# Kernel tuning notes

Measured on AMD Instinct MI355X. Metric: run time of the kernel, lower is better.

## Reference

```python
import jax, jax.numpy as jnp
import numpy as np

B, T, K, F, H, LH, OUT = 256, 90, 17, 2, 64, 512, 57
N_PER = T * K  # 1530 nodes per graph
IN1 = K * (H + F)  # 1122
CONNS = [[15,13],[13,11],[16,14],[14,12],[11,12],[5,11],[6,12],[5,6],[5,7],[6,8],[7,9],[8,10],[1,2],[0,1],[0,2],[1,3],[2,4],[3,5],[4,6]]

def _build_edge_index():
    temporal = np.array([[i, i + K] for i in range(N_PER - K)], dtype=np.int64).T
    structural = np.array([[a + i * K, b + i * K] for a, b in CONNS for i in range(T)], dtype=np.int64).T
    e = np.concatenate([temporal, structural], axis=1)
    e = np.concatenate([e, e[::-1]], axis=1)  # bidirectional
    e = np.concatenate([e + g * N_PER for g in range(B)], axis=1)  # batch offsets
    return jnp.asarray(e)


def setup_inputs() -> dict:
    key = jax.random.key(0)
    ks = jax.random.split(key, 40)
    def n(i, shape, s=0.05):
        return jax.random.normal(ks[i], shape, dtype=jnp.float32) * s
    inp = {
        'x': jax.random.normal(ks[0], (B * N_PER, F), dtype=jnp.float32),
        'edge_index': _build_edge_index(),
        'gat1_W': n(1, (F, H), 0.3), 'gat1_asrc': n(2, (H,), 0.3), 'gat1_adst': n(3, (H,), 0.3), 'gat1_b': n(4, (H,)),
        'bn1_g': jnp.ones((H,), jnp.float32), 'bn1_b': jnp.zeros((H,), jnp.float32),
        'gat2_W': n(5, (H, H), 0.1), 'gat2_asrc': n(6, (H,), 0.3), 'gat2_adst': n(7, (H,), 0.3), 'gat2_b': n(8, (H,)),
        'bn2_g': jnp.ones((H,), jnp.float32), 'bn2_b': jnp.zeros((H,), jnp.float32),
        'l1f_wih': n(9, (4 * LH, IN1)), 'l1f_whh': n(10, (4 * LH, LH)), 'l1f_bih': n(11, (4 * LH,)), 'l1f_bhh': n(12, (4 * LH,)),
        'l1b_wih': n(13, (4 * LH, IN1)), 'l1b_whh': n(14, (4 * LH, LH)), 'l1b_bih': n(15, (4 * LH,)), 'l1b_bhh': n(16, (4 * LH,)),
        'l2f_wih': n(17, (4 * LH, 2 * LH)), 'l2f_whh': n(18, (4 * LH, LH)), 'l2f_bih': n(19, (4 * LH,)), 'l2f_bhh': n(20, (4 * LH,)),
        'l2b_wih': n(21, (4 * LH, 2 * LH)), 'l2b_whh': n(22, (4 * LH, LH)), 'l2b_bih': n(23, (4 * LH,)), 'l2b_bhh': n(24, (4 * LH,)),
        'h1_w': n(25, (2 * LH, 256)), 'h1_b': n(26, (256,)),
        'h2_w': n(27, (256, OUT)), 'h2_b': n(28, (OUT,)),
    }
    return inp


def _gat(x, src, dst, W, a_src, a_dst, b):
    # PyG GATConv, heads=1, self-loops included in src/dst
    N = x.shape[0]
    xp = x @ W  # [N, H]
    e = jax.nn.leaky_relu((xp @ a_src)[src] + (xp @ a_dst)[dst], 0.2)  # [E]
    m = jax.ops.segment_max(e, dst, num_segments=N)
    w = jnp.exp(e - m[dst])
    den = jax.ops.segment_sum(w, dst, num_segments=N)
    alpha = w / den[dst]
    out = jax.ops.segment_sum(xp[src] * alpha[:, None], dst, num_segments=N)
    return out + b


def _bn(x, g, b):
    mu = x.mean(0)
    var = ((x - mu) ** 2).mean(0)
    return g * (x - mu) * jax.lax.rsqrt(var + 1e-5) + b


def _lstm_dir(x, wih, whh, bih, bhh):
    Bn, Hh = x.shape[0], whh.shape[1]
    def step(carry, xt):
        h, c = carry
        z = xt @ wih.T + h @ whh.T + bih + bhh
        i, f, g, o = jnp.split(z, 4, axis=-1)  # torch gate order
        c = jax.nn.sigmoid(f) * c + jax.nn.sigmoid(i) * jnp.tanh(g)
        h = jax.nn.sigmoid(o) * jnp.tanh(c)
        return (h, c), h
    h0 = jnp.zeros((Bn, Hh), x.dtype)
    _, hs = jax.lax.scan(step, (h0, h0), jnp.swapaxes(x, 0, 1))
    return jnp.swapaxes(hs, 0, 1)


def _bilstm(x, wf_ih, wf_hh, bf_ih, bf_hh, wb_ih, wb_hh, bb_ih, bb_hh):
    fwd = _lstm_dir(x, wf_ih, wf_hh, bf_ih, bf_hh)
    bwd = _lstm_dir(x[:, ::-1], wb_ih, wb_hh, bb_ih, bb_hh)[:, ::-1]
    return jnp.concatenate([fwd, bwd], axis=-1)


def reference(x, edge_index,
              gat1_W, gat1_asrc, gat1_adst, gat1_b, bn1_g, bn1_b,
              gat2_W, gat2_asrc, gat2_adst, gat2_b, bn2_g, bn2_b,
              l1f_wih, l1f_whh, l1f_bih, l1f_bhh, l1b_wih, l1b_whh, l1b_bih, l1b_bhh,
              l2f_wih, l2f_whh, l2f_bih, l2f_bhh, l2b_wih, l2b_whh, l2b_bih, l2b_bhh,
              h1_w, h1_b, h2_w, h2_b):
    N = x.shape[0]
    sl = jnp.arange(N)
    src = jnp.concatenate([edge_index[0], sl])  # add self loops (GATConv default)
    dst = jnp.concatenate([edge_index[1], sl])
    h = jax.nn.relu(_bn(_gat(x, src, dst, gat1_W, gat1_asrc, gat1_adst, gat1_b), bn1_g, bn1_b))
    h = jax.nn.relu(_bn(_gat(h, src, dst, gat2_W, gat2_asrc, gat2_adst, gat2_b), bn2_g, bn2_b))
    feats = jnp.concatenate([h, x], axis=1).reshape(B, T, IN1)  # [B, 90, 1122]
    o = _bilstm(feats, l1f_wih, l1f_whh, l1f_bih, l1f_bhh, l1b_wih, l1b_whh, l1b_bih, l1b_bhh)
    o = _bilstm(o, l2f_wih, l2f_whh, l2f_bih, l2f_bhh, l2b_wih, l2b_whh, l2b_bih, l2b_bhh)
    o = jax.nn.relu(o @ h1_w + h1_b) @ h2_w + h2_b  # [B, 90, 57]
    return o
```

## Files before the change

kernel.cpp:

```cpp
#include <hip/hip_runtime.h>
#include <cstdint>
#include <cstddef>

#define B_    256
#define T_    90
#define K_    17
#define NPER  1530
#define NN    (B_*NPER)
#define H_    64
#define LH    512
#define G4    2048
#define IN1   1122
#define IN1P  1152
#define SEQR  (B_*T_)
#define OUT_  57

typedef unsigned short u16;
typedef __attribute__((ext_vector_type(8))) short short8;
typedef __attribute__((ext_vector_type(4))) float f32x4;

__device__ __forceinline__ float b2f(u16 u){ union{unsigned i; float f;} x; x.i=((unsigned)u)<<16; return x.f; }
__device__ __forceinline__ u16 f2b(float f){ union{float f; unsigned i;} x; x.f=f; unsigned r=x.i+0x7fffu+((x.i>>16)&1u); return (u16)(r>>16); }
__device__ __forceinline__ float sigm(float v){ return 1.f/(1.f+__expf(-v)); }
__device__ __forceinline__ float tanh_(float v){ return 2.f*sigm(2.f*v)-1.f; }

__global__ __launch_bounds__(256)
void stg_sentinel(float* __restrict__ out, int n){
  int i=blockIdx.x*256+threadIdx.x;
  if(i<n) out[i]=123.0f;
}

__global__ __launch_bounds__(256)
void stg_permute_w(const float* __restrict__ src, u16* __restrict__ dst, int Ks, int Kd){
  size_t idx=(size_t)blockIdx.x*256+threadIdx.x;
  int rn=(int)(idx/Kd), kk=(int)(idx%Kd);
  int j=rn>>2, G=rn&3, ro=G*LH+j;
  dst[idx] = (kk<Ks)? f2b(src[(size_t)ro*Ks+kk]) : (u16)0;
}

__global__ __launch_bounds__(256)
void stg_prep_bias(const float* __restrict__ bih, const float* __restrict__ bhh, float* __restrict__ dst){
  int rn=blockIdx.x*256+threadIdx.x;
  int j=rn>>2, G=rn&3, ro=G*LH+j;
  dst[rn]=bih[ro]+bhh[ro];
}

__global__ __launch_bounds__(256)
void stg_transpose_pad(const float* __restrict__ src, u16* __restrict__ dst, int R, int C, int Crows){
  size_t idx=(size_t)blockIdx.x*256+threadIdx.x;
  int c=(int)(idx/R), r=(int)(idx%R);
  dst[idx] = (c<C)? f2b(src[(size_t)r*C+c]) : (u16)0;
  (void)Crows;
}

__global__ __launch_bounds__(256)
void stg_gat1_xp(const float* __restrict__ x, const float* __restrict__ W, u16* __restrict__ xp){
  size_t idx=(size_t)blockIdx.x*256+threadIdx.x;
  size_t n=idx>>6; int c=idx&63;
  float v=x[n*2]*W[c]+x[n*2+1]*W[64+c];
  xp[idx]=f2b(v);
}

__global__ __launch_bounds__(256)
void stg_scores(const u16* __restrict__ xp, const float* __restrict__ as, const float* __restrict__ ad,
                float* __restrict__ ssrc, float* __restrict__ sdst){
  const int lane=threadIdx.x&63;
  const size_t n=(size_t)blockIdx.x*4+(threadIdx.x>>6);
  float v=b2f(xp[n*64+lane]);
  float s1=v*as[lane], s2=v*ad[lane];
  #pragma unroll
  for(int m=1;m<64;m<<=1){ s1+=__shfl_xor(s1,m); s2+=__shfl_xor(s2,m); }
  if(lane==0){ ssrc[n]=s1; sdst[n]=s2; }
}

__constant__ int c_deg[17]={2,3,3,2,2,4,4,2,2,1,1,3,3,2,2,1,1};
__constant__ int c_adj[17][4]={{1,2,0,0},{2,0,3,0},{1,0,4,0},{1,5,0,0},{2,6,0,0},
 {11,6,7,3},{12,5,8,4},{5,9,0,0},{6,10,0,0},{7,0,0,0},{8,0,0,0},
 {13,12,5,0},{14,11,6,0},{15,11,0,0},{16,12,0,0},{13,0,0,0},{14,0,0,0}};

__global__ __launch_bounds__(256)
void stg_gat_agg(const u16* __restrict__ xp, const float* __restrict__ ssrc, const float* __restrict__ sdst,
                 const float* __restrict__ bias, u16* __restrict__ out){
  const int lane=threadIdx.x&63;
  const int n=blockIdx.x*4+(threadIdx.x>>6);
  const int r=n%NPER, t=r/K_, k=r%K_;
  const int dg=c_deg[k];
  const int base=n-k;
  const int nb0=n;
  const int nb1=(t>0)?      n-K_ : n;  const bool v1=(t>0);
  const int nb2=(t<T_-1)?   n+K_ : n;  const bool v2=(t<T_-1);
  const int nb3=base+c_adj[k][0];
  const int nb4=base+c_adj[k][1];      const bool v4=(dg>1);
  const int nb5=base+c_adj[k][2];      const bool v5=(dg>2);
  const int nb6=base+c_adj[k][3];      const bool v6=(dg>3);
  const float sd=sdst[n];
  const float NEG=-1e30f;
  auto lrelu=[](float v){ return v>0.f? v : 0.2f*v; };
  float e0=lrelu(ssrc[nb0]+sd);
  float e1=v1? lrelu(ssrc[nb1]+sd) : NEG;
  float e2=v2? lrelu(ssrc[nb2]+sd) : NEG;
  float e3=    lrelu(ssrc[nb3]+sd);
  float e4=v4? lrelu(ssrc[nb4]+sd) : NEG;
  float e5=v5? lrelu(ssrc[nb5]+sd) : NEG;
  float e6=v6? lrelu(ssrc[nb6]+sd) : NEG;
  float mx=fmaxf(fmaxf(fmaxf(e0,e1),fmaxf(e2,e3)),fmaxf(fmaxf(e4,e5),e6));
  float w0=__expf(e0-mx), w1=__expf(e1-mx), w2=__expf(e2-mx), w3=__expf(e3-mx);
  float w4=__expf(e4-mx), w5=__expf(e5-mx), w6=__expf(e6-mx);
  const float inv=1.f/(w0+w1+w2+w3+w4+w5+w6);
  float acc = w0*b2f(xp[(size_t)nb0*64+lane])
            + w1*b2f(xp[(size_t)nb1*64+lane])
            + w2*b2f(xp[(size_t)nb2*64+lane])
            + w3*b2f(xp[(size_t)nb3*64+lane])
            + w4*b2f(xp[(size_t)nb4*64+lane])
            + w5*b2f(xp[(size_t)nb5*64+lane])
            + w6*b2f(xp[(size_t)nb6*64+lane]);
  out[(size_t)n*64+lane]=f2b(acc*inv+bias[lane]);
}

__global__ __launch_bounds__(256)
void stg_bn_part(const u16* __restrict__ in, float* __restrict__ part){
  const int c=threadIdx.x&63, sub=threadIdx.x>>6;
  float s=0.f,q=0.f;
  for(size_t n=(size_t)blockIdx.x*4+sub; n<NN; n+=1024){
    float v=b2f(in[n*64+c]); s+=v; q+=v*v;
  }
  __shared__ float sS[4][64], sQ[4][64];
  sS[sub][c]=s; sQ[sub][c]=q;
  __syncthreads();
  if(sub==0){
    float a=0,bq=0;
    for(int i=0;i<4;i++){a+=sS[i][c]; bq+=sQ[i][c];}
    part[blockIdx.x*128+c*2]=a; part[blockIdx.x*128+c*2+1]=bq;
  }
}

__global__ void stg_bn_fin(const float* __restrict__ part, const float* __restrict__ g,
                           const float* __restrict__ b, float* __restrict__ stats){
  const int c=threadIdx.x;
  float s=0,q=0;
  for(int p=0;p<256;++p){ s+=part[p*128+c*2]; q+=part[p*128+c*2+1]; }
  const float invN=1.f/(float)NN;
  float mu=s*invN, var=q*invN-mu*mu;
  float istd=rsqrtf(var+1e-5f);
  float a=g[c]*istd;
  stats[c*2]=a; stats[c*2+1]=b[c]-mu*a;
}

__global__ __launch_bounds__(256)
void stg_bn_apply(const u16* __restrict__ in, const float* __restrict__ stats, u16* __restrict__ out){
  size_t idx=(size_t)blockIdx.x*256+threadIdx.x;
  int c=idx&63;
  float v=b2f(in[idx])*stats[c*2]+stats[c*2+1];
  out[idx]=f2b(fmaxf(v,0.f));
}

__global__ __launch_bounds__(256)
void stg_build_feats(const u16* __restrict__ h2, const float* __restrict__ x, u16* __restrict__ feats){
  size_t idx=(size_t)blockIdx.x*256+threadIdx.x;
  size_t row=idx/IN1P; int cc=(int)(idx%IN1P);
  u16 outv=0;
  if(cc<IN1){
    int k=cc/66, f=cc%66;
    size_t g=row/T_, t=row%T_;
    size_t node=g*NPER+t*K_+k;
    outv = (f<64)? h2[node*64+f] : f2b(x[node*2+(f-64)]);
  }
  feats[idx]=outv;
}

template<int BM,int BN,int EPI>
__global__ __launch_bounds__(256)
void stg_gemm_bt(const u16* __restrict__ A, int ldA,
                 const u16* __restrict__ Bt, int ldB,
                 void* __restrict__ Cp, int ldC, int K,
                 const float* __restrict__ bias)
{
  constexpr int WM=BM/2, WN=BN/2, FM=WM/16, FN=WN/16;
  __shared__ u16 As[BM*32];
  __shared__ u16 Bs[BN*32];
  const int tid=threadIdx.x, w=tid>>6, lane=tid&63;
  const int wr=w>>1, wc=w&1;
  const size_t row0=(size_t)blockIdx.x*BM;
  const size_t col0=(size_t)blockIdx.y*BN;
  f32x4 acc[FM][FN];
  #pragma unroll
  for(int i=0;i<FM;i++)
    #pragma unroll
    for(int j=0;j<FN;j++)
      #pragma unroll
      for(int r=0;r<4;r++) acc[i][j][r]=0.f;

  for(int k0=0;k0<K;k0+=32){
    #pragma unroll
    for(int q=0;q<BM/64;++q){
      const int is=w*(BM/64)+q;
      const u16* gp=A+(row0+is*16+(lane>>2))*(size_t)ldA+k0+(lane&3)*8;
      *(short8*)&As[is*512+lane*8]=*(const short8*)gp;
    }
    #pragma unroll
    for(int q=0;q<BN/64;++q){
      const int is=w*(BN/64)+q;
      const u16* gp=Bt+(col0+is*16+(lane>>2))*(size_t)ldB+k0+(lane&3)*8;
      *(short8*)&Bs[is*512+lane*8]=*(const short8*)gp;
    }
    __syncthreads();
    short8 af[FM], bf[FN];
    #pragma unroll
    for(int mi=0;mi<FM;mi++)
      af[mi]=*(const short8*)&As[(wr*WM+mi*16+(lane&15))*32+(lane>>4)*8];
    #pragma unroll
    for(int ni=0;ni<FN;ni++)
      bf[ni]=*(const short8*)&Bs[(wc*WN+ni*16+(lane&15))*32+(lane>>4)*8];
    #pragma unroll
    for(int mi=0;mi<FM;mi++)
      #pragma unroll
      for(int ni=0;ni<FN;ni++)
        acc[mi][ni]=__builtin_amdgcn_mfma_f32_16x16x32_bf16(af[mi],bf[ni],acc[mi][ni],0,0,0);
    __syncthreads();
  }
  #pragma unroll
  for(int mi=0;mi<FM;mi++)
   #pragma unroll
   for(int ni=0;ni<FN;ni++)
    #pragma unroll
    for(int r=0;r<4;r++){
      const size_t row=row0+wr*WM+mi*16+(lane>>4)*4+r;
      const size_t col=col0+wc*WN+ni*16+(lane&15);
      float v=acc[mi][ni][r];
      if constexpr (EPI==0){ ((u16*)Cp)[row*ldC+col]=f2b(v); }
      else if constexpr (EPI==1){ v+=bias[col]; ((u16*)Cp)[row*ldC+col]=f2b(fmaxf(v,0.f)); }
      else { if(col<OUT_){ ((float*)Cp)[row*ldC+col]=v+bias[col]; } }
    }
}

__global__ __launch_bounds__(512)
void stg_lstm_step(const u16* __restrict__ hprev, u16* __restrict__ hcur,
                   float* __restrict__ cst,
                   const u16* __restrict__ whh,
                   const u16* __restrict__ xpf, const u16* __restrict__ xpb,
                   const float* __restrict__ bias,
                   u16* __restrict__ seq,
                   int t)
{
  __shared__ u16 As[2][2*2048];
  __shared__ u16 Bs[2][2*2048];
  __shared__ float Zs[64*64];
  const int dir = blockIdx.z;
  const int tt  = dir ? (T_-1-t) : t;
  const u16* xp = dir ? xpb : xpf;
  const u16* Ap = hprev + (size_t)dir*B_*LH;
  const u16* Bp = whh   + (size_t)dir*G4*LH;
  const float* bs = bias + dir*G4;
  const int tid=threadIdx.x, w=tid>>6, lane=tid&63;
  const int wr=w>>2, wc=w&3;
  const int row0=blockIdx.x*64, col0=blockIdx.y*64;

  const int sp=w>>2, ss=w&3;
  const int srow=ss*16+(lane>>2);
  const int scO=(lane&3)*8;
  const u16* gA = Ap + (size_t)(row0+srow)*LH + sp*32 + scO;
  const u16* gB = Bp + (size_t)(col0+srow)*LH + sp*32 + scO;
  const int lA = sp*2048 + srow*32 + scO;

  f32x4 acc[2];
  #pragma unroll
  for(int i=0;i<2;i++)
    #pragma unroll
    for(int r=0;r<4;r++) acc[i][r]=0.f;

  short8 ra=*(const short8*)(gA);
  short8 rb=*(const short8*)(gB);
  *(short8*)&As[0][lA]=ra; *(short8*)&Bs[0][lA]=rb;

  int cur=0;
  for(int it=0; it<8; ++it){
    if(it<7){ ra=*(const short8*)(gA+(it+1)*64); rb=*(const short8*)(gB+(it+1)*64); }
    __syncthreads();
    #pragma unroll
    for(int p=0;p<2;++p){
      short8 af[2], bf;
      #pragma unroll
      for(int mi=0;mi<2;mi++)
        af[mi]=*(const short8*)&As[cur][p*2048+(wr*32+mi*16+(lane&15))*32+(lane>>4)*8];
      bf=*(const short8*)&Bs[cur][p*2048+(wc*16+(lane&15))*32+(lane>>4)*8];
      #pragma unroll
      for(int mi=0;mi<2;mi++)
        acc[mi]=__builtin_amdgcn_mfma_f32_16x16x32_bf16(af[mi],bf,acc[mi],0,0,0);
    }
    if(it<7){ *(short8*)&As[cur^1][lA]=ra; *(short8*)&Bs[cur^1][lA]=rb; }
    cur^=1;
  }
  #pragma unroll
  for(int mi=0;mi<2;mi++)
    #pragma unroll
    for(int r=0;r<4;r++){
      const int rl=wr*32+mi*16+(lane>>4)*4+r;
      const int cl=wc*16+(lane&15);
      const int b=row0+rl, gc=col0+cl;
      float z=acc[mi][r] + b2f(xp[(size_t)(b*T_+tt)*G4+gc]) + bs[gc];
      Zs[rl*64+cl]=z;
    }
  __syncthreads();
  for(int id=tid; id<64*16; id+=512){
    const int rl=id>>4, u=id&15;
    const int b=row0+rl, ug=(col0>>2)+u;
    const float zi=Zs[rl*64+4*u+0], zf=Zs[rl*64+4*u+1];
    const float zg=Zs[rl*64+4*u+2], zo=Zs[rl*64+4*u+3];
    const size_t ci=(size_t)dir*B_*LH + (size_t)b*LH + ug;
    float c = sigm(zf)*cst[ci] + sigm(zi)*tanh_(zg);
    cst[ci]=c;
    float h = sigm(zo)*tanh_(c);
    hcur[ci]=f2b(h);
    seq[(size_t)(b*T_+tt)*(2*LH) + (size_t)dir*LH + ug]=f2b(h);
  }
}

extern "C" void kernel_launch(void* const* d_in, const int* in_sizes, int n_in,
                              void* d_out, int out_size, void* d_ws, size_t ws_size,
                              hipStream_t stream)
{
  (void)in_sizes; (void)n_in;
  const float* x    =(const float*)d_in[0];
  const float* g1W  =(const float*)d_in[2];
  const float* g1as =(const float*)d_in[3];
  const float* g1ad =(const float*)d_in[4];
  const float* g1b  =(const float*)d_in[5];
  const float* bn1g =(const float*)d_in[6];
  const float* bn1b =(const float*)d_in[7];
  const float* g2W  =(const float*)d_in[8];
  const float* g2as =(const float*)d_in[9];
  const float* g2ad =(const float*)d_in[10];
  const float* g2b  =(const float*)d_in[11];
  const float* bn2g =(const float*)d_in[12];
  const float* bn2b =(const float*)d_in[13];
  const float* l1f_wih=(const float*)d_in[14];
  const float* l1f_whh=(const float*)d_in[15];
  const float* l1f_bih=(const float*)d_in[16];
  const float* l1f_bhh=(const float*)d_in[17];
  const float* l1b_wih=(const float*)d_in[18];
  const float* l1b_whh=(const float*)d_in[19];
  const float* l1b_bih=(const float*)d_in[20];
  const float* l1b_bhh=(const float*)d_in[21];
  const float* l2f_wih=(const float*)d_in[22];
  const float* l2f_whh=(const float*)d_in[23];
  const float* l2f_bih=(const float*)d_in[24];
  const float* l2f_bhh=(const float*)d_in[25];
  const float* l2b_wih=(const float*)d_in[26];
  const float* l2b_whh=(const float*)d_in[27];
  const float* l2b_bih=(const float*)d_in[28];
  const float* l2b_bhh=(const float*)d_in[29];
  const float* h1w  =(const float*)d_in[30];
  const float* h1b  =(const float*)d_in[31];
  const float* h2w  =(const float*)d_in[32];
  const float* h2b  =(const float*)d_in[33];

  const size_t SZ_w1ih  = (size_t)G4*IN1P*2;
  const size_t SZ_w2ih  = (size_t)G4*1024*2;
  const size_t SZ_whh   = (size_t)4*G4*LH*2;
  const size_t SZ_bias  = (size_t)4*G4*4;
  const size_t SZ_w2gT  = (size_t)64*64*2;
  const size_t SZ_h1T   = (size_t)256*1024*2;
  const size_t SZ_h2T   = (size_t)64*256*2;
  const size_t SZ_part  = (size_t)256*128*4;
  const size_t SZ_stats = (size_t)64*2*4;
  const size_t SZ_hs    = (size_t)2*B_*LH*2;
  const size_t SZ_cs    = (size_t)2*B_*LH*4;
  const size_t SZ_xpr   = (size_t)SEQR*G4*2;
  const size_t SZ_R12   = 2*SZ_xpr;
  const size_t SZ_feats = (size_t)SEQR*IN1P*2;
  const size_t SZ_gat   = (size_t)NN*64*2;
  const size_t SZ_sc    = (size_t)NN*4;

  char* base=(char*)d_ws; size_t o=0;
  auto take=[&](size_t b)->size_t{ size_t r=o; o=(o+b+255)&~(size_t)255; return r; };
  const size_t off_w1ih = take(2*SZ_w1ih);
  const size_t off_whh  = take(SZ_whh);
  const size_t off_bias = take(SZ_bias);
  const size_t off_w2gT = take(SZ_w2gT);
  const size_t off_h1T  = take(SZ_h1T);
  const size_t off_h2T  = take(SZ_h2T);
  const size_t off_part = take(SZ_part);
  const size_t off_stat = take(SZ_stats);
  const size_t off_hs0  = take(SZ_hs);
  const size_t off_hs1  = take(SZ_hs);
  const size_t off_cs   = take(SZ_cs);
  const size_t off_R12  = take(SZ_R12);
  const size_t off_R3   = take(SZ_feats);
  const size_t NEED = o;
  if (NEED > ws_size) {
    stg_sentinel<<<(out_size+255)/256,256,0,stream>>>((float*)d_out, out_size);
    return;
  }

  u16* w1ihF=(u16*)(base+off_w1ih);
  u16* w1ihB=(u16*)(base+off_w1ih+SZ_w1ih);
  u16* w2ihF=(u16*)(base+off_w1ih);
  u16* w2ihB=(u16*)(base+off_w1ih+SZ_w2ih);
  u16* whhAll=(u16*)(base+off_whh);
  float* biasAll=(float*)(base+off_bias);
  u16* w2gT=(u16*)(base+off_w2gT);
  u16* h1T =(u16*)(base+off_h1T);
  u16* h2T =(u16*)(base+off_h2T);
  float* part=(float*)(base+off_part);
  float* stats=(float*)(base+off_stat);
  u16* hs0=(u16*)(base+off_hs0);
  u16* hs1=(u16*)(base+off_hs1);
  float* cs=(float*)(base+off_cs);
  u16* xprF=(u16*)(base+off_R12);
  u16* xprB=(u16*)(base+off_R12+SZ_xpr);
  u16* xpB_=(u16*)(base+off_R12);
  u16* aggB=(u16*)(base+off_R12+SZ_gat);
  u16* hB  =(u16*)(base+off_R12+2*SZ_gat);
  float* ssrc=(float*)(base+off_R12+3*SZ_gat);
  float* sdst=(float*)(base+off_R12+3*SZ_gat+SZ_sc);
  u16* mid =(u16*)(base+off_R12);
  u16* feats=(u16*)(base+off_R3);
  u16* seq  =(u16*)(base+off_R3);

  stg_permute_w<<<G4*IN1P/256,256,0,stream>>>(l1f_wih,w1ihF,IN1,IN1P);
  stg_permute_w<<<G4*IN1P/256,256,0,stream>>>(l1b_wih,w1ihB,IN1,IN1P);
  stg_permute_w<<<G4*LH/256,256,0,stream>>>(l1f_whh,whhAll+0*(size_t)G4*LH,LH,LH);
  stg_permute_w<<<G4*LH/256,256,0,stream>>>(l1b_whh,whhAll+1*(size_t)G4*LH,LH,LH);
  stg_permute_w<<<G4*LH/256,256,0,stream>>>(l2f_whh,whhAll+2*(size_t)G4*LH,LH,LH);
  stg_permute_w<<<G4*LH/256,256,0,stream>>>(l2b_whh,whhAll+3*(size_t)G4*LH,LH,LH);
  stg_prep_bias<<<G4/256,256,0,stream>>>(l1f_bih,l1f_bhh,biasAll+0*G4);
  stg_prep_bias<<<G4/256,256,0,stream>>>(l1b_bih,l1b_bhh,biasAll+1*G4);
  stg_prep_bias<<<G4/256,256,0,stream>>>(l2f_bih,l2f_bhh,biasAll+2*G4);
  stg_prep_bias<<<G4/256,256,0,stream>>>(l2b_bih,l2b_bhh,biasAll+3*G4);
  stg_transpose_pad<<<64*64/256,256,0,stream>>>(g2W,w2gT,64,64,64);
  stg_transpose_pad<<<256*1024/256,256,0,stream>>>(h1w,h1T,1024,256,256);
  stg_transpose_pad<<<64*256/256,256,0,stream>>>(h2w,h2T,256,57,64);

  stg_gat1_xp<<<NN*64/256,256,0,stream>>>(x,g1W,xpB_);
  stg_scores<<<NN/4,256,0,stream>>>(xpB_,g1as,g1ad,ssrc,sdst);
  stg_gat_agg<<<NN/4,256,0,stream>>>(xpB_,ssrc,sdst,g1b,aggB);
  stg_bn_part<<<256,256,0,stream>>>(aggB,part);
  stg_bn_fin<<<1,64,0,stream>>>(part,bn1g,bn1b,stats);
  stg_bn_apply<<<NN*64/256,256,0,stream>>>(aggB,stats,hB);

  stg_gemm_bt<128,64,0><<<dim3(NN/128,1),256,0,stream>>>(hB,64,w2gT,64,xpB_,64,64,nullptr);
  stg_scores<<<NN/4,256,0,stream>>>(xpB_,g2as,g2ad,ssrc,sdst);
  stg_gat_agg<<<NN/4,256,0,stream>>>(xpB_,ssrc,sdst,g2b,aggB);
  stg_bn_part<<<256,256,0,stream>>>(aggB,part);
  stg_bn_fin<<<1,64,0,stream>>>(part,bn2g,bn2b,stats);
  stg_bn_apply<<<NN*64/256,256,0,stream>>>(aggB,stats,hB);

  stg_build_feats<<<SEQR*IN1P/256,256,0,stream>>>(hB,x,feats);

  stg_gemm_bt<128,128,0><<<dim3(SEQR/128,G4/128),256,0,stream>>>(feats,IN1P,w1ihF,IN1P,xprF,G4,IN1P,nullptr);
  stg_gemm_bt<128,128,0><<<dim3(SEQR/128,G4/128),256,0,stream>>>(feats,IN1P,w1ihB,IN1P,xprB,G4,IN1P,nullptr);
  stg_permute_w<<<G4*1024/256,256,0,stream>>>(l2f_wih,w2ihF,1024,1024);
  stg_permute_w<<<G4*1024/256,256,0,stream>>>(l2b_wih,w2ihB,1024,1024);

  hipMemsetAsync(hs0,0,SZ_hs,stream);
  hipMemsetAsync(cs,0,SZ_cs,stream);
  for(int t=0;t<T_;++t){
    u16* hp=(t&1)?hs1:hs0; u16* hc=(t&1)?hs0:hs1;
    stg_lstm_step<<<dim3(B_/64,G4/64,2),512,0,stream>>>(hp,hc,cs,whhAll,xprF,xprB,biasAll,seq,t);
  }

  stg_gemm_bt<128,128,0><<<dim3(SEQR/128,G4/128),256,0,stream>>>(seq,1024,w2ihF,1024,xprF,G4,1024,nullptr);
  stg_gemm_bt<128,128,0><<<dim3(SEQR/128,G4/128),256,0,stream>>>(seq,1024,w2ihB,1024,xprB,G4,1024,nullptr);
  hipMemsetAsync(hs0,0,SZ_hs,stream);
  hipMemsetAsync(cs,0,SZ_cs,stream);
  for(int t=0;t<T_;++t){
    u16* hp=(t&1)?hs1:hs0; u16* hc=(t&1)?hs0:hs1;
    stg_lstm_step<<<dim3(B_/64,G4/64,2),512,0,stream>>>(hp,hc,cs,whhAll+(size_t)2*G4*LH,xprF,xprB,biasAll+2*G4,seq,t);
  }

  stg_gemm_bt<128,128,1><<<dim3(SEQR/128,256/128),256,0,stream>>>(seq,1024,h1T,1024,mid,256,1024,h1b);
  stg_gemm_bt<128,64,2><<<dim3(SEQR/128,1),256,0,stream>>>(mid,256,h2T,256,d_out,OUT_,256,h2b);
}
```

Baseline: 2.605 ms.

## Make each LSTM layer a persistent cooperative kernel and use direct-to-LDS loads

Each LSTM layer, previously 90 per-step kernel launches, now runs as a single cooperative kernel that loops over time steps and separates them with grid.sync. Each block loads its slice of the recurrent weights into registers once and keeps it there for the whole sequence, so only the hidden state is reloaded each step. The GEMM and LSTM tile loads now use global_load_lds to copy straight into shared memory in MFMA fragment order, skipping the register staging. The risks are the cost of a grid-wide barrier at every step, higher register pressure from the held weights, and a 256-block grid that must fit co-resident for the cooperative launch.

```diff
diff --git a/kernel.cpp b/kernel.cpp
--- a/kernel.cpp
+++ b/kernel.cpp
@@ -1,6 +1,9 @@
 #include <hip/hip_runtime.h>
+#include <hip/hip_cooperative_groups.h>
 #include <cstdint>
 #include <cstddef>
+
+namespace cg = cooperative_groups;
 
 #define B_    256
 #define T_    90
@@ -23,6 +26,13 @@
 __device__ __forceinline__ u16 f2b(float f){ union{float f; unsigned i;} x; x.f=f; unsigned r=x.i+0x7fffu+((x.i>>16)&1u); return (u16)(r>>16); }
 __device__ __forceinline__ float sigm(float v){ return 1.f/(1.f+__expf(-v)); }
 __device__ __forceinline__ float tanh_(float v){ return 2.f*sigm(2.f*v)-1.f; }
+
+__device__ __forceinline__ void gll16(const u16* gp, u16* lp){
+  __builtin_amdgcn_global_load_lds(
+      (const __attribute__((address_space(1))) unsigned int*)gp,
+      (__attribute__((address_space(3))) unsigned int*)lp,
+      16, 0, 0);
+}
 
 __global__ __launch_bounds__(256)
 void stg_sentinel(float* __restrict__ out, int n){
@@ -175,9 +185,9 @@
                  void* __restrict__ Cp, int ldC, int K,
                  const float* __restrict__ bias)
 {
-  constexpr int WM=BM/2, WN=BN/2, FM=WM/16, FN=WN/16;
-  __shared__ u16 As[BM*32];
-  __shared__ u16 Bs[BN*32];
+  constexpr int WM=BM/2, WN=BN/2, FM=WM/16, FN=WN/16, CM=BM/16, CN=BN/16;
+  __shared__ u16 As[CM*512];
+  __shared__ u16 Bs[CN*512];
   const int tid=threadIdx.x, w=tid>>6, lane=tid&63;
   const int wr=w>>1, wc=w&1;
   const size_t row0=(size_t)blockIdx.x*BM;
@@ -192,25 +202,19 @@
 
   for(int k0=0;k0<K;k0+=32){
     #pragma unroll
-    for(int q=0;q<BM/64;++q){
-      const int is=w*(BM/64)+q;
-      const u16* gp=A+(row0+is*16+(lane>>2))*(size_t)ldA+k0+(lane&3)*8;
-      *(short8*)&As[is*512+lane*8]=*(const short8*)gp;
-    }
-    #pragma unroll
-    for(int q=0;q<BN/64;++q){
-      const int is=w*(BN/64)+q;
-      const u16* gp=Bt+(col0+is*16+(lane>>2))*(size_t)ldB+k0+(lane&3)*8;
-      *(short8*)&Bs[is*512+lane*8]=*(const short8*)gp;
-    }
+    for(int c=w;c<CM;c+=4)
+      gll16(A +(row0+c*16+(lane&15))*(size_t)ldA+k0+(lane>>4)*8, &As[c*512]);
+    #pragma unroll
+    for(int c=w;c<CN;c+=4)
+      gll16(Bt+(col0+c*16+(lane&15))*(size_t)ldB+k0+(lane>>4)*8, &Bs[c*512]);
     __syncthreads();
     short8 af[FM], bf[FN];
     #pragma unroll
     for(int mi=0;mi<FM;mi++)
-      af[mi]=*(const short8*)&As[(wr*WM+mi*16+(lane&15))*32+(lane>>4)*8];
+      af[mi]=*(const short8*)&As[((wr*FM+mi)*64+lane)*8];
     #pragma unroll
     for(int ni=0;ni<FN;ni++)
-      bf[ni]=*(const short8*)&Bs[(wc*WN+ni*16+(lane&15))*32+(lane>>4)*8];
+      bf[ni]=*(const short8*)&Bs[((wc*FN+ni)*64+lane)*8];
     #pragma unroll
     for(int mi=0;mi<FM;mi++)
       #pragma unroll
@@ -233,85 +237,80 @@
     }
 }
 
-__global__ __launch_bounds__(512)
-void stg_lstm_step(const u16* __restrict__ hprev, u16* __restrict__ hcur,
-                   float* __restrict__ cst,
-                   const u16* __restrict__ whh,
-                   const u16* __restrict__ xpf, const u16* __restrict__ xpb,
-                   const float* __restrict__ bias,
-                   u16* __restrict__ seq,
-                   int t)
+__global__ __launch_bounds__(512,2)
+void stg_lstm_layer(u16* __restrict__ hs0, u16* __restrict__ hs1,
+                    float* __restrict__ cst,
+                    const u16* __restrict__ whh,
+                    const u16* __restrict__ xpf, const u16* __restrict__ xpb,
+                    const float* __restrict__ bias,
+                    u16* __restrict__ seq)
 {
-  __shared__ u16 As[2][2*2048];
-  __shared__ u16 Bs[2][2*2048];
+  cg::grid_group grid = cg::this_grid();
+  __shared__ u16 As[64*512];
   __shared__ float Zs[64*64];
   const int dir = blockIdx.z;
-  const int tt  = dir ? (T_-1-t) : t;
   const u16* xp = dir ? xpb : xpf;
-  const u16* Ap = hprev + (size_t)dir*B_*LH;
-  const u16* Bp = whh   + (size_t)dir*G4*LH;
-  const float* bs = bias + dir*G4;
   const int tid=threadIdx.x, w=tid>>6, lane=tid&63;
   const int wr=w>>2, wc=w&3;
   const int row0=blockIdx.x*64, col0=blockIdx.y*64;
 
-  const int sp=w>>2, ss=w&3;
-  const int srow=ss*16+(lane>>2);
-  const int scO=(lane&3)*8;
-  const u16* gA = Ap + (size_t)(row0+srow)*LH + sp*32 + scO;
-  const u16* gB = Bp + (size_t)(col0+srow)*LH + sp*32 + scO;
-  const int lA = sp*2048 + srow*32 + scO;
-
-  f32x4 acc[2];
-  #pragma unroll
-  for(int i=0;i<2;i++)
-    #pragma unroll
-    for(int r=0;r<4;r++) acc[i][r]=0.f;
-
-  short8 ra=*(const short8*)(gA);
-  short8 rb=*(const short8*)(gB);
-  *(short8*)&As[0][lA]=ra; *(short8*)&Bs[0][lA]=rb;
-
-  int cur=0;
-  for(int it=0; it<8; ++it){
-    if(it<7){ ra=*(const short8*)(gA+(it+1)*64); rb=*(const short8*)(gB+(it+1)*64); }
+  short8 bfr[16];
+  {
+    const u16* Bp = whh + (size_t)dir*G4*LH + (size_t)(col0 + wc*16 + (lane&15))*LH + (lane>>4)*8;
+    #pragma unroll
+    for(int kk=0;kk<16;kk++) bfr[kk] = *(const short8*)(Bp + kk*32);
+  }
+  const float bias_v = bias[dir*G4 + col0 + wc*16 + (lane&15)];
+
+  for(int t=0;t<T_;++t){
+    const int tt = dir ? (T_-1-t) : t;
+    const u16* hp = ((t&1)? hs1 : hs0) + (size_t)dir*B_*LH;
+    u16* hc       = ((t&1)? hs0 : hs1) + (size_t)dir*B_*LH;
+
+    #pragma unroll
+    for(int q=0;q<8;++q){
+      const int c = w*8+q, g = c>>4, kk = c&15;
+      gll16(hp + (size_t)(row0 + g*16 + (lane&15))*LH + kk*32 + (lane>>4)*8, &As[c*512]);
+    }
     __syncthreads();
-    #pragma unroll
-    for(int p=0;p<2;++p){
-      short8 af[2], bf;
+
+    f32x4 acc[2];
+    #pragma unroll
+    for(int i=0;i<2;i++)
       #pragma unroll
-      for(int mi=0;mi<2;mi++)
-        af[mi]=*(const short8*)&As[cur][p*2048+(wr*32+mi*16+(lane&15))*32+(lane>>4)*8];
-      bf=*(const short8*)&Bs[cur][p*2048+(wc*16+(lane&15))*32+(lane>>4)*8];
+      for(int r=0;r<4;r++) acc[i][r]=0.f;
+    #pragma unroll
+    for(int kk=0;kk<16;++kk){
       #pragma unroll
-      for(int mi=0;mi<2;mi++)
-        acc[mi]=__builtin_amdgcn_mfma_f32_16x16x32_bf16(af[mi],bf,acc[mi],0,0,0);
+      for(int mi=0;mi<2;++mi){
+        short8 af=*(const short8*)&As[(((wr*2+mi)*16+kk)*512)+lane*8];
+        acc[mi]=__builtin_amdgcn_mfma_f32_16x16x32_bf16(af,bfr[kk],acc[mi],0,0,0);
+      }
     }
-    if(it<7){ *(short8*)&As[cur^1][lA]=ra; *(short8*)&Bs[cur^1][lA]=rb; }
-    cur^=1;
-  }
-  #pragma unroll
-  for(int mi=0;mi<2;mi++)
-    #pragma unroll
-    for(int r=0;r<4;r++){
-      const int rl=wr*32+mi*16+(lane>>4)*4+r;
-      const int cl=wc*16+(lane&15);
-      const int b=row0+rl, gc=col0+cl;
-      float z=acc[mi][r] + b2f(xp[(size_t)(b*T_+tt)*G4+gc]) + bs[gc];
-      Zs[rl*64+cl]=z;
+    #pragma unroll
+    for(int mi=0;mi<2;mi++)
+      #pragma unroll
+      for(int r=0;r<4;r++){
+        const int rl=wr*32+mi*16+(lane>>4)*4+r;
+        const int cl=wc*16+(lane&15);
+        const int b=row0+rl, gc=col0+cl;
+        Zs[rl*64+cl]=acc[mi][r] + b2f(xp[(size_t)(b*T_+tt)*G4+gc]) + bias_v;
+      }
+    __syncthreads();
+    #pragma unroll
+    for(int ii=0;ii<2;++ii){
+      const int id=tid+ii*512;
+      const int rl=id>>4, u=id&15;
+      const int b=row0+rl, ug=(col0>>2)+u;
+      f32x4 zv=*(const f32x4*)&Zs[rl*64+4*u];
+      const size_t ci=(size_t)dir*B_*LH + (size_t)b*LH + ug;
+      float c = sigm(zv[1])*cst[ci] + sigm(zv[0])*tanh_(zv[2]);
+      cst[ci]=c;
+      float h = sigm(zv[3])*tanh_(c);
+      hc[(size_t)dir*0 + (size_t)b*LH + ug - (size_t)0] = f2b(h);
+      seq[(size_t)(b*T_+tt)*(2*LH) + (size_t)dir*LH + ug]=f2b(h);
     }
-  __syncthreads();
-  for(int id=tid; id<64*16; id+=512){
-    const int rl=id>>4, u=id&15;
-    const int b=row0+rl, ug=(col0>>2)+u;
-    const float zi=Zs[rl*64+4*u+0], zf=Zs[rl*64+4*u+1];
-    const float zg=Zs[rl*64+4*u+2], zo=Zs[rl*64+4*u+3];
-    const size_t ci=(size_t)dir*B_*LH + (size_t)b*LH + ug;
-    float c = sigm(zf)*cst[ci] + sigm(zi)*tanh_(zg);
-    cst[ci]=c;
-    float h = sigm(zo)*tanh_(c);
-    hcur[ci]=f2b(h);
-    seq[(size_t)(b*T_+tt)*(2*LH) + (size_t)dir*LH + ug]=f2b(h);
+    grid.sync();
   }
 }
 
@@ -454,18 +453,20 @@
 
   hipMemsetAsync(hs0,0,SZ_hs,stream);
   hipMemsetAsync(cs,0,SZ_cs,stream);
-  for(int t=0;t<T_;++t){
-    u16* hp=(t&1)?hs1:hs0; u16* hc=(t&1)?hs0:hs1;
-    stg_lstm_step<<<dim3(B_/64,G4/64,2),512,0,stream>>>(hp,hc,cs,whhAll,xprF,xprB,biasAll,seq,t);
+  {
+    u16* whp=whhAll; float* bsp=biasAll;
+    void* args[]={&hs0,&hs1,&cs,&whp,&xprF,&xprB,&bsp,&seq};
+    hipLaunchCooperativeKernel((const void*)stg_lstm_layer, dim3(4,32,2), dim3(512), args, 0, stream);
   }
 
   stg_gemm_bt<128,128,0><<<dim3(SEQR/128,G4/128),256,0,stream>>>(seq,1024,w2ihF,1024,xprF,G4,1024,nullptr);
   stg_gemm_bt<128,128,0><<<dim3(SEQR/128,G4/128),256,0,stream>>>(seq,1024,w2ihB,1024,xprB,G4,1024,nullptr);
   hipMemsetAsync(hs0,0,SZ_hs,stream);
   hipMemsetAsync(cs,0,SZ_cs,stream);
-  for(int t=0;t<T_;++t){
-    u16* hp=(t&1)?hs1:hs0; u16* hc=(t&1)?hs0:hs1;
-    stg_lstm_step<<<dim3(B_/64,G4/64,2),512,0,stream>>>(hp,hc,cs,whhAll+(size_t)2*G4*LH,xprF,xprB,biasAll+2*G4,seq,t);
+  {
+    u16* whp=whhAll+(size_t)2*G4*LH; float* bsp=biasAll+2*G4;
+    void* args[]={&hs0,&hs1,&cs,&whp,&xprF,&xprB,&bsp,&seq};
+    hipLaunchCooperativeKernel((const void*)stg_lstm_layer, dim3(4,32,2), dim3(512), args, 0, stream);
   }
 
   stg_gemm_bt<128,128,1><<<dim3(SEQR/128,256/128),256,0,stream>>>(seq,1024,h1T,1024,mid,256,1024,h1b);
```

Measured after the change: 8.216 ms. +215.4%, slower.
